# Kernel tuning notes

Measured on AMD Instinct MI355X. Metric: run time of the kernel, lower is better.

Reference implementation:

```python
import jax, jax.numpy as jnp
import numpy as np

B, IN_DIM, EXP_DIM, E = 16384, 256, 128, 8  # batch, input_dim, expert_dim, expert_num


def setup_inputs() -> dict:
    key = jax.random.key(0)
    ks = jax.random.split(key, 12)
    s_in = 1.0 / np.sqrt(IN_DIM)
    return {
        "x_a": jax.random.normal(ks[0], (B, IN_DIM), jnp.float32),
        "x_b": jax.random.normal(ks[1], (B, IN_DIM), jnp.float32),
        "x_share": jax.random.normal(ks[2], (B, IN_DIM), jnp.float32),
        # expert banks: [E, IN_DIM, EXP_DIM] weights, [E, EXP_DIM] bias
        "Wa": jax.random.uniform(ks[3], (E, IN_DIM, EXP_DIM), jnp.float32, -s_in, s_in),
        "ba": jax.random.uniform(ks[4], (E, EXP_DIM), jnp.float32, -s_in, s_in),
        "Wb": jax.random.uniform(ks[5], (E, IN_DIM, EXP_DIM), jnp.float32, -s_in, s_in),
        "bb": jax.random.uniform(ks[6], (E, EXP_DIM), jnp.float32, -s_in, s_in),
        "Ws": jax.random.uniform(ks[7], (E, IN_DIM, EXP_DIM), jnp.float32, -s_in, s_in),
        "bs": jax.random.uniform(ks[8], (E, EXP_DIM), jnp.float32, -s_in, s_in),
        # gate projections (bias=False): num single-output linears == one [num, IN_DIM] matrix
        "Ga": jax.random.uniform(ks[9], (2 * E, IN_DIM), jnp.float32, -s_in, s_in),
        "Gb": jax.random.uniform(ks[10], (2 * E, IN_DIM), jnp.float32, -s_in, s_in),
        "Gs": jax.random.uniform(ks[11], (3 * E, IN_DIM), jnp.float32, -s_in, s_in),
    }


def _experts(x, W, b):
    # batched dense stack: [B,IN] x [E,IN,D] -> [B,E,D]
    return jnp.einsum("bi,eid->bed", x, W) + b[None, :, :]


def _gate(x, G, experts):
    # logits [B, num]; softmax over experts; weighted sum over expert axis
    w = jax.nn.softmax(x @ G.T, axis=1)
    return jnp.einsum("be,bed->bd", w, experts)


def reference(x_a, x_b, x_share, Wa, ba, Wb, bb, Ws, bs, Ga, Gb, Gs):
    ea = _experts(x_a, Wa, ba)          # [B,E,D]
    eb = _experts(x_b, Wb, bb)          # [B,E,D]
    es = _experts(x_share, Ws, bs)      # [B,E,D]
    out_a = _gate(x_a, Ga, jnp.concatenate([ea, es], axis=1))
    out_b = _gate(x_b, Gb, jnp.concatenate([eb, es], axis=1))
    out_s = _gate(x_share, Gs, jnp.concatenate([ea, eb, es], axis=1))
    return (out_a, out_b, out_s)
```

## Files before the change

kernel.cpp:

```cpp
#include <hip/hip_runtime.h>
#include <stdint.h>

#define BATCH 16384
#define INDIM 256
#define DDIM  128
#define NEXP  8
#define ROWS  64

typedef __bf16 bfv8  __attribute__((ext_vector_type(8)));
typedef float  f32x4 __attribute__((ext_vector_type(4)));

__global__ void prep_kernel(const float* __restrict__ Wa, const float* __restrict__ Wb,
                            const float* __restrict__ Ws, const float* __restrict__ Ga,
                            const float* __restrict__ Gb, const float* __restrict__ Gs,
                            __bf16* __restrict__ wp, __bf16* __restrict__ gp) {
    int t = blockIdx.x * 256 + threadIdx.x;
    const int NW = 3 * 8 * 8 * 8 * 64;
    if (t < NW) {
        int lane = t & 63, nt = (t >> 6) & 7, kt = (t >> 9) & 7, e = (t >> 12) & 7, st = t >> 15;
        const float* W = (st == 0) ? Wa : (st == 1) ? Wb : Ws;
        int d  = nt * 16 + (lane & 15);
        int i0 = kt * 32 + (lane >> 4) * 8;
        __bf16* o = wp + (size_t)t * 8;
#pragma unroll
        for (int j = 0; j < 8; j++)
            o[j] = (__bf16)W[(size_t)(e * 256 + i0 + j) * 128 + d];
    } else if (t < NW + 2048) {
        int t2 = t - NW;
        int lane = t2 & 63, nt = (t2 >> 6) & 3, kt = t2 >> 8;
        int g  = nt * 16 + (lane & 15);
        int k0 = kt * 32 + (lane >> 4) * 8;
        __bf16* o = gp + (size_t)t2 * 8;
#pragma unroll
        for (int j = 0; j < 8; j++) {
            int k = k0 + j;
            float v = 0.f;
            if (g < 16)      v = Ga[g * 256 + k];
            else if (g < 32) v = Gb[(g - 16) * 256 + k];
            else if (g < 56) v = Gs[(g - 32) * 256 + k];
            o[j] = (__bf16)v;
        }
    }
}

__device__ __forceinline__ void load_afr(const float* __restrict__ x, int rb,
                                         int l16, int quad, bfv8 afr[2][8]) {
#pragma unroll
    for (int mt = 0; mt < 2; mt++) {
        const float* xr = x + (size_t)(rb + mt * 16 + l16) * INDIM;
#pragma unroll
        for (int kt = 0; kt < 8; kt++) {
            f32x4 lo = *(const f32x4*)(xr + kt * 32 + quad * 8);
            f32x4 hi = *(const f32x4*)(xr + kt * 32 + quad * 8 + 4);
            bfv8 a;
            a[0] = (__bf16)lo[0]; a[1] = (__bf16)lo[1]; a[2] = (__bf16)lo[2]; a[3] = (__bf16)lo[3];
            a[4] = (__bf16)hi[0]; a[5] = (__bf16)hi[1]; a[6] = (__bf16)hi[2]; a[7] = (__bf16)hi[3];
            afr[mt][kt] = a;
        }
    }
}

__device__ __forceinline__ void async_load16(const __bf16* g, __bf16* l) {
    __builtin_amdgcn_global_load_lds(
        (const __attribute__((address_space(1))) uint32_t*)g,
        (__attribute__((address_space(3))) uint32_t*)l, 16, 0, 0);
}

__launch_bounds__(640, 2)
__global__ void ple_kernel(const float* __restrict__ xa, const float* __restrict__ xb,
                           const float* __restrict__ xs,
                           const float* __restrict__ ba, const float* __restrict__ bb,
                           const float* __restrict__ bs,
                           const __bf16* __restrict__ wp, const __bf16* __restrict__ gp,
                           float* __restrict__ out) {
    __shared__ __bf16 Bbuf[2][32768];
    __shared__ float  wT[64 * ROWS];
    __shared__ int    ready[24];
    __shared__ int    done[24];

    const int tid  = threadIdx.x;
    const int w    = tid >> 6;
    const int lane = tid & 63;
    const int quad = lane >> 4;
    const int l16  = lane & 15;
    const int r0   = blockIdx.x * ROWS;

    float* lgt = (float*)&Bbuf[0][0];

    if (tid < 24) { ready[tid] = 0; done[tid] = 0; }

    if (w < 8) {
        const int nt = w >> 1;
        const int mh = (w & 1) * 32;
        const float* x = (nt == 0) ? xa : (nt == 1) ? xb : xs;
        bfv8 afr[2][8];
        load_afr(x, r0 + mh, l16, quad, afr);
        f32x4 acc0 = {0.f, 0.f, 0.f, 0.f}, acc1 = {0.f, 0.f, 0.f, 0.f};
#pragma unroll
        for (int kt = 0; kt < 8; kt++) {
            bfv8 g = *(const bfv8*)(gp + ((size_t)(kt * 4 + nt) * 64 + lane) * 8);
            acc0 = __builtin_amdgcn_mfma_f32_16x16x32_bf16(afr[0][kt], g, acc0, 0, 0, 0);
            acc1 = __builtin_amdgcn_mfma_f32_16x16x32_bf16(afr[1][kt], g, acc1, 0, 0, 0);
        }
#pragma unroll
        for (int r = 0; r < 4; r++) {
            lgt[(mh + quad * 4 + r) * 64 + nt * 16 + l16]      = acc0[r];
            lgt[(mh + 16 + quad * 4 + r) * 64 + nt * 16 + l16] = acc1[r];
        }
    }
    __syncthreads();

    if (tid < ROWS) {
        const float* L = lgt + tid * 64;
#pragma unroll
        for (int gi = 0; gi < 3; gi++) {
            const int base = (gi == 0) ? 0 : (gi == 1 ? 16 : 32);
            const int cnt  = (gi == 2) ? 24 : 16;
            float m = -1e30f;
            for (int k = 0; k < cnt; k++) m = fmaxf(m, L[base + k]);
            float s = 0.f;
            for (int k = 0; k < cnt; k++) s += __expf(L[base + k] - m);
            float inv = 1.f / s;
            for (int k = 0; k < cnt; k++) wT[(base + k) * ROWS + tid] = __expf(L[base + k] - m) * inv;
        }
    }
    __syncthreads();

    if (w >= 8) {
        const int pid = w - 8;
#pragma unroll 1
        for (int g = pid; g < 24; g += 2) {
            if (g >= 2) {
                while (__hip_atomic_load(&done[g - 2], __ATOMIC_ACQUIRE,
                                         __HIP_MEMORY_SCOPE_WORKGROUP) < 8)
                    __builtin_amdgcn_s_sleep(2);
            }
            const __bf16* gsrc = wp + (size_t)g * 32768 + (size_t)lane * 8;
            __bf16* ldst = &Bbuf[g & 1][0];
#pragma unroll
            for (int c = 0; c < 64; c++)
                async_load16(gsrc + (size_t)c * 512, ldst + c * 512);
            __asm__ volatile("s_waitcnt vmcnt(0)" ::: "memory");
            __hip_atomic_store(&ready[g], 1, __ATOMIC_RELEASE,
                               __HIP_MEMORY_SCOPE_WORKGROUP);
        }
        return;
    }

    const int wr = w >> 2;
    const int wc = w & 3;
    const int mb = wr * 32;

    float o[3][2][2][4];
#pragma unroll
    for (int oi = 0; oi < 3; oi++)
#pragma unroll
        for (int mt = 0; mt < 2; mt++)
#pragma unroll
            for (int ntl = 0; ntl < 2; ntl++)
#pragma unroll
                for (int r = 0; r < 4; r++) o[oi][mt][ntl][r] = 0.f;

#define FOLD(oi, gbase)                                                                \
    {                                                                                  \
        _Pragma("unroll")                                                              \
        for (int mt = 0; mt < 2; mt++) {                                               \
            f32x4 wv = *(const f32x4*)(wT + (gbase + eb) * ROWS + mb + mt * 16 + quad * 4); \
            _Pragma("unroll")                                                          \
            for (int ntl = 0; ntl < 2; ntl++)                                          \
                _Pragma("unroll")                                                      \
                for (int r = 0; r < 4; r++)                                            \
                    o[oi][mt][ntl][r] += wv[r] * acc[mt][ntl][r];                      \
        }                                                                              \
    }

    bfv8 afr[2][8];

#pragma unroll 1
    for (int g = 0; g < 24; g++) {
        const int st = g >> 3;
        const int eb = g & 7;
        if ((g & 7) == 0) {
            const float* x = (st == 0) ? xa : (st == 1) ? xb : xs;
            load_afr(x, r0 + mb, l16, quad, afr);
        }
        while (__hip_atomic_load(&ready[g], __ATOMIC_ACQUIRE,
                                 __HIP_MEMORY_SCOPE_WORKGROUP) == 0)
            __builtin_amdgcn_s_sleep(1);

        const __bf16* bbase = &Bbuf[g & 1][0] + (size_t)(2 * wc) * 512 + (size_t)lane * 8;

        f32x4 acc[2][2];
#pragma unroll
        for (int mt = 0; mt < 2; mt++)
#pragma unroll
            for (int ntl = 0; ntl < 2; ntl++) { f32x4 z = {0.f, 0.f, 0.f, 0.f}; acc[mt][ntl] = z; }

#pragma unroll
        for (int kt = 0; kt < 8; kt++) {
            bfv8 c0 = *(const bfv8*)(bbase + (size_t)kt * 4096);
            bfv8 c1 = *(const bfv8*)(bbase + (size_t)kt * 4096 + 512);
            acc[0][0] = __builtin_amdgcn_mfma_f32_16x16x32_bf16(afr[0][kt], c0, acc[0][0], 0, 0, 0);
            acc[1][0] = __builtin_amdgcn_mfma_f32_16x16x32_bf16(afr[1][kt], c0, acc[1][0], 0, 0, 0);
            acc[0][1] = __builtin_amdgcn_mfma_f32_16x16x32_bf16(afr[0][kt], c1, acc[0][1], 0, 0, 0);
            acc[1][1] = __builtin_amdgcn_mfma_f32_16x16x32_bf16(afr[1][kt], c1, acc[1][1], 0, 0, 0);
        }

        if (lane == 0)
            __hip_atomic_fetch_add(&done[g], 1, __ATOMIC_RELEASE,
                                   __HIP_MEMORY_SCOPE_WORKGROUP);

        const float* bias = (st == 0) ? ba : (st == 1) ? bb : bs;
        float b0 = bias[eb * 128 + wc * 32 + l16];
        float b1 = bias[eb * 128 + wc * 32 + 16 + l16];
#pragma unroll
        for (int mt = 0; mt < 2; mt++)
#pragma unroll
            for (int r = 0; r < 4; r++) { acc[mt][0][r] += b0; acc[mt][1][r] += b1; }

        if (st == 0)      { FOLD(0, 0);  FOLD(2, 32); }
        else if (st == 1) { FOLD(1, 16); FOLD(2, 40); }
        else              { FOLD(0, 8);  FOLD(1, 24); FOLD(2, 48); }
    }
#undef FOLD

#pragma unroll
    for (int oi = 0; oi < 3; oi++) {
        float* ob = out + (size_t)oi * BATCH * DDIM;
#pragma unroll
        for (int mt = 0; mt < 2; mt++)
#pragma unroll
            for (int r = 0; r < 4; r++) {
                int row = r0 + mb + mt * 16 + quad * 4 + r;
#pragma unroll
                for (int ntl = 0; ntl < 2; ntl++)
                    ob[(size_t)row * DDIM + wc * 32 + ntl * 16 + l16] = o[oi][mt][ntl][r];
            }
    }
}

extern "C" void kernel_launch(void* const* d_in, const int* in_sizes, int n_in,
                              void* d_out, int out_size, void* d_ws, size_t ws_size,
                              hipStream_t stream) {
    const float* xa = (const float*)d_in[0];
    const float* xb = (const float*)d_in[1];
    const float* xs = (const float*)d_in[2];
    const float* Wa = (const float*)d_in[3];
    const float* ba = (const float*)d_in[4];
    const float* Wb = (const float*)d_in[5];
    const float* bb = (const float*)d_in[6];
    const float* Ws = (const float*)d_in[7];
    const float* bs = (const float*)d_in[8];
    const float* Ga = (const float*)d_in[9];
    const float* Gb = (const float*)d_in[10];
    const float* Gs = (const float*)d_in[11];

    __bf16* wp = (__bf16*)d_ws;
    __bf16* gp = wp + 3 * 8 * 8 * 8 * 64 * 8;

    prep_kernel<<<392, 256, 0, stream>>>(Wa, Wb, Ws, Ga, Gb, Gs, wp, gp);
    ple_kernel<<<BATCH / ROWS, 640, 0, stream>>>(xa, xb, xs, ba, bb, bs, wp, gp, (float*)d_out);
}
```

Before: 194.2 us.

## Replace producer-warp spin-wait pipeline with cooperative double-buffered prefetch and barriers

Drops the two dedicated loader warps and the ready/done atomic flag handshake. All eight compute warps now issue async global-to-LDS loads for the next expert slice into the other buffer before computing the current one, with a workgroup barrier at the end of each stage. The gate-logit scratch moves to the second buffer so stage 0 can be prefetched during the softmax. This removes spin-wait polling and extra warps, but adds a full barrier per stage. It also relies on the barrier to cover completion of the async LDS writes.

```diff
diff --git a/kernel.cpp b/kernel.cpp
--- a/kernel.cpp
+++ b/kernel.cpp
@@ -66,7 +66,7 @@
         (__attribute__((address_space(3))) uint32_t*)l, 16, 0, 0);
 }
 
-__launch_bounds__(640, 2)
+__launch_bounds__(512, 2)
 __global__ void ple_kernel(const float* __restrict__ xa, const float* __restrict__ xb,
                            const float* __restrict__ xs,
                            const float* __restrict__ ba, const float* __restrict__ bb,
@@ -75,8 +75,6 @@
                            float* __restrict__ out) {
     __shared__ __bf16 Bbuf[2][32768];
     __shared__ float  wT[64 * ROWS];
-    __shared__ int    ready[24];
-    __shared__ int    done[24];
 
     const int tid  = threadIdx.x;
     const int w    = tid >> 6;
@@ -85,15 +83,14 @@
     const int l16  = lane & 15;
     const int r0   = blockIdx.x * ROWS;
 
-    float* lgt = (float*)&Bbuf[0][0];
-
-    if (tid < 24) { ready[tid] = 0; done[tid] = 0; }
-
-    if (w < 8) {
+    float* lgt = (float*)&Bbuf[1][0];
+
+    bfv8 afr[2][8];
+
+    {
         const int nt = w >> 1;
         const int mh = (w & 1) * 32;
         const float* x = (nt == 0) ? xa : (nt == 1) ? xb : xs;
-        bfv8 afr[2][8];
         load_afr(x, r0 + mh, l16, quad, afr);
         f32x4 acc0 = {0.f, 0.f, 0.f, 0.f}, acc1 = {0.f, 0.f, 0.f, 0.f};
 #pragma unroll
@@ -109,6 +106,14 @@
         }
     }
     __syncthreads();
+
+    {
+        const __bf16* src = wp + (size_t)w * 4096 + (size_t)lane * 8;
+        __bf16* dst = &Bbuf[0][w * 4096];
+#pragma unroll
+        for (int c = 0; c < 8; c++)
+            async_load16(src + (size_t)c * 512, dst + c * 512);
+    }
 
     if (tid < ROWS) {
         const float* L = lgt + tid * 64;
@@ -125,27 +130,6 @@
         }
     }
     __syncthreads();
-
-    if (w >= 8) {
-        const int pid = w - 8;
-#pragma unroll 1
-        for (int g = pid; g < 24; g += 2) {
-            if (g >= 2) {
-                while (__hip_atomic_load(&done[g - 2], __ATOMIC_ACQUIRE,
-                                         __HIP_MEMORY_SCOPE_WORKGROUP) < 8)
-                    __builtin_amdgcn_s_sleep(2);
-            }
-            const __bf16* gsrc = wp + (size_t)g * 32768 + (size_t)lane * 8;
-            __bf16* ldst = &Bbuf[g & 1][0];
-#pragma unroll
-            for (int c = 0; c < 64; c++)
-                async_load16(gsrc + (size_t)c * 512, ldst + c * 512);
-            __asm__ volatile("s_waitcnt vmcnt(0)" ::: "memory");
-            __hip_atomic_store(&ready[g], 1, __ATOMIC_RELEASE,
-                               __HIP_MEMORY_SCOPE_WORKGROUP);
-        }
-        return;
-    }
 
     const int wr = w >> 2;
     const int wc = w & 3;
@@ -174,22 +158,26 @@
         }                                                                              \
     }
 
-    bfv8 afr[2][8];
-
 #pragma unroll 1
     for (int g = 0; g < 24; g++) {
         const int st = g >> 3;
         const int eb = g & 7;
-        if ((g & 7) == 0) {
+
+        if (eb == 0) {
             const float* x = (st == 0) ? xa : (st == 1) ? xb : xs;
             load_afr(x, r0 + mb, l16, quad, afr);
         }
-        while (__hip_atomic_load(&ready[g], __ATOMIC_ACQUIRE,
-                                 __HIP_MEMORY_SCOPE_WORKGROUP) == 0)
-            __builtin_amdgcn_s_sleep(1);
-
-        const __bf16* bbase = &Bbuf[g & 1][0] + (size_t)(2 * wc) * 512 + (size_t)lane * 8;
-
+
+        if (g < 23) {
+            const __bf16* src = wp + (size_t)(g + 1) * 32768 + (size_t)w * 4096
+                                + (size_t)lane * 8;
+            __bf16* dst = &Bbuf[(g + 1) & 1][w * 4096];
+#pragma unroll
+            for (int c = 0; c < 8; c++)
+                async_load16(src + (size_t)c * 512, dst + c * 512);
+        }
+
+        const __bf16* bbase = &Bbuf[g & 1][(2 * wc) * 512] + (size_t)lane * 8;
         f32x4 acc[2][2];
 #pragma unroll
         for (int mt = 0; mt < 2; mt++)
@@ -206,10 +194,6 @@
             acc[1][1] = __builtin_amdgcn_mfma_f32_16x16x32_bf16(afr[1][kt], c1, acc[1][1], 0, 0, 0);
         }
 
-        if (lane == 0)
-            __hip_atomic_fetch_add(&done[g], 1, __ATOMIC_RELEASE,
-                                   __HIP_MEMORY_SCOPE_WORKGROUP);
-
         const float* bias = (st == 0) ? ba : (st == 1) ? bb : bs;
         float b0 = bias[eb * 128 + wc * 32 + l16];
         float b1 = bias[eb * 128 + wc * 32 + 16 + l16];
@@ -221,6 +205,8 @@
         if (st == 0)      { FOLD(0, 0);  FOLD(2, 32); }
         else if (st == 1) { FOLD(1, 16); FOLD(2, 40); }
         else              { FOLD(0, 8);  FOLD(1, 24); FOLD(2, 48); }
+
+        __syncthreads();
     }
 #undef FOLD
 
@@ -259,5 +245,5 @@
     __bf16* gp = wp + 3 * 8 * 8 * 8 * 64 * 8;
 
     prep_kernel<<<392, 256, 0, stream>>>(Wa, Wb, Ws, Ga, Gb, Gs, wp, gp);
-    ple_kernel<<<BATCH / ROWS, 640, 0, stream>>>(xa, xb, xs, ba, bb, bs, wp, gp, (float*)d_out);
-}
+    ple_kernel<<<BATCH / ROWS, 512, 0, stream>>>(xa, xb, xs, ba, bb, bs, wp, gp, (float*)d_out);
+}
```

New measurement: 176.4 us. -9.2%, faster.
